# Kernel optimization log

Measured on AMD Instinct MI355X. Metric: run time of the kernel, lower is better.

Reference implementation:

```python
import jax, jax.numpy as jnp
import numpy as np

S = 1            # support_num
NEIGHBOR = 32    # neighbor_num for ball query
EPS = 1e-12

def _gather(t, idx):
    # t: (bs, N, C), idx: (bs, M, n) -> (bs, M, n, C)
    return jax.vmap(lambda tb, ib: tb[ib])(t, idx)

def _pick(t, idx):
    # t: (bs, M, C), idx: (bs, V) -> (bs, V, C)
    return jax.vmap(lambda tb, ib: tb[ib])(t, idx)

def _normalize(x, axis):
    return x / jnp.maximum(jnp.linalg.norm(x, axis=axis, keepdims=True), EPS)

def query_ball_point(radius, nsample, xyz, new_xyz):
    # PointNet++-style ball query: indices of first nsample points within radius,
    # missing slots filled with the first valid neighbor (self, since dist=0).
    sq = jnp.sum((new_xyz[:, :, None, :] - xyz[:, None, :, :]) ** 2, axis=-1)  # (bs,S,N)
    N = xyz.shape[1]
    idx = jnp.broadcast_to(jnp.arange(N), sq.shape)
    idx = jnp.where(sq > radius * radius, N, idx)
    idx = jnp.sort(idx, axis=-1)[:, :, :nsample]
    return jnp.where(idx == N, idx[:, :, :1], idx)

def _dir_norm(vertices, nbr_idx):
    nbrs = _gather(vertices, nbr_idx)                       # (bs,v,n,3)
    return _normalize(nbrs - vertices[:, :, None, :], axis=-1)

def conv_surface(nbr_idx, vertices, directions, K=32):
    # directions: (3, S*K)
    dn = _dir_norm(vertices, nbr_idx)
    theta = jax.nn.relu(jnp.einsum('bvnd,dk->bvnk', dn, _normalize(directions, 0)))
    bs, v, n, _ = theta.shape
    return theta.reshape(bs, v, n, S, K).max(axis=2).sum(axis=2)  # (bs,v,K)

def conv_layer(nbr_idx, vertices, fm, w, b, d, K=32):
    # w: (Cin,(S+1)*K), b: ((S+1)*K,), d: (3,S*K)
    dn = _dir_norm(vertices, nbr_idx)
    theta = jax.nn.relu(jnp.einsum('bvnd,dk->bvnk', dn, _normalize(d, 0)))  # (bs,v,n,S*K)
    f = jnp.einsum('bvc,ck->bvk', fm, w) + b                # (bs,v,(S+1)*K)
    center, support = f[..., :K], f[..., K:]
    sup = _gather(support, nbr_idx)                          # (bs,v,n,S*K)
    bs, v, n, _ = sup.shape
    act = (theta * sup).reshape(bs, v, n, S, K).max(axis=2).sum(axis=2)
    return center + act

def pool_layer(vertices, fm, radius, key, rate=4, nn_num=4):
    idx = query_ball_point(radius, nn_num, vertices, vertices)
    pooled = _gather(fm, idx).max(axis=2)                    # neighborhood max-pool
    v = vertices.shape[1]
    perm = jax.random.permutation(key, v)[: v // rate]       # random subsample (fixed key)
    return vertices[:, perm], pooled[:, perm]

def get_nearest_index(target, source):
    sq = jnp.sum((target[:, :, None, :] - source[:, None, :, :]) ** 2, axis=-1)
    return jnp.argmin(sq, axis=-1)                           # (bs, V_target)

def _forward(vertices, onehot, d0, w1, b1, dd1, w2, b2, dd2, w3, b3, dd3,
             w4, b4, dd4, w5, b5, dd5, w6, b6, dd6, w7, b7, dd7,
             cw1, cb1, cw2, cb2, cw3, cb3):
    relu = jax.nn.relu
    bs, V, _ = vertices.shape
    ni = query_ball_point(0.25, NEIGHBOR, vertices, vertices)
    fm0 = relu(conv_surface(ni, vertices, d0))
    fm1 = jnp.concatenate([fm0, relu(conv_layer(ni, vertices, fm0, w1, b1, dd1))], -1)
    fm2 = jnp.concatenate([fm1, relu(conv_layer(ni, vertices, fm1, w2, b2, dd2))], -1)
    v1, fp1 = pool_layer(vertices, fm2, 0.25, jax.random.fold_in(jax.random.key(42), 1))
    ni = query_ball_point(0.39, NEIGHBOR, v1, v1)
    fm3 = jnp.concatenate([fp1, relu(conv_layer(ni, v1, fp1, w3, b3, dd3))], -1)
    fm4 = jnp.concatenate([fm3, relu(conv_layer(ni, v1, fm3, w4, b4, dd4))], -1)
    fm5 = jnp.concatenate([fm4, relu(conv_layer(ni, v1, fm4, w5, b5, dd5))], -1)
    v2, fp2 = pool_layer(v1, fm5, 0.39, jax.random.fold_in(jax.random.key(42), 2))
    ni = query_ball_point(0.63, NEIGHBOR, v2, v2)
    fm6 = jnp.concatenate([fp2, relu(conv_layer(ni, v2, fp2, w6, b6, dd6))], -1)
    fm7 = jnp.concatenate([fm6, relu(conv_layer(ni, v2, fm6, w7, b7, dd7))], -1)
    f_global = fm7.max(axis=1)                               # (bs, 256)
    n1 = get_nearest_index(vertices, v1)
    n2 = get_nearest_index(vertices, v2)
    fuse = jnp.concatenate([
        fm0, fm1, fm2,
        _pick(fm3, n1), _pick(fm4, n1), _pick(fm5, n1),
        _pick(fm6, n2), _pick(fm7, n2),
        jnp.broadcast_to(f_global[:, None, :], (bs, V, f_global.shape[-1])),
        jnp.broadcast_to(onehot[:, None, :], (bs, V, onehot.shape[-1])),
    ], axis=-1)                                              # (bs, V, 1424)
    h = relu(jnp.einsum('bvc,oc->bvo', fuse, cw1) + cb1)
    h = relu(jnp.einsum('bvc,oc->bvo', h, cw2) + cb2)
    return jnp.einsum('bvc,oc->bvo', h, cw3) + cb3           # (bs, V, class_num)


def setup_inputs() -> dict:
    key = jax.random.key(0)
    ks = iter(jax.random.split(key, 40))
    bs, N, cat = 8, 2048, 16
    vertices = jax.random.uniform(next(ks), (bs, N, 3), dtype=jnp.float32)
    labels = jax.random.randint(next(ks), (bs,), 0, cat)
    onehot = jax.nn.one_hot(labels, cat, dtype=jnp.float32)
    def p(shape):
        return jax.random.normal(next(ks), shape, dtype=jnp.float32) * 0.05
    inp = {"vertices": vertices, "onehot": onehot, "d0": p((3, S * 32))}
    ins = [32, 64, 96, 128, 160, 192, 224]
    for i, c in enumerate(ins, start=1):
        inp[f"w{i}"] = p((c, (S + 1) * 32))
        inp[f"b{i}"] = p(((S + 1) * 32,))
        inp[f"dd{i}"] = p((3, S * 32))
    inp["cw1"] = p((1024, 1424)); inp["cb1"] = p((1024,))
    inp["cw2"] = p((512, 1024)); inp["cb2"] = p((512,))
    inp["cw3"] = p((50, 512)); inp["cb3"] = p((50,))
    return inp


def reference(vertices, onehot, d0, w1, b1, dd1, w2, b2, dd2, w3, b3, dd3,
              w4, b4, dd4, w5, b5, dd5, w6, b6, dd6, w7, b7, dd7,
              cw1, cb1, cw2, cb2, cw3, cb3):
    return _forward(vertices, onehot, d0, w1, b1, dd1, w2, b2, dd2, w3, b3, dd3,
                    w4, b4, dd4, w5, b5, dd5, w6, b6, dd6, w7, b7, dd7,
                    cw1, cb1, cw2, cb2, cw3, cb3)
```

## Files before the change

### kernel.cpp

```cpp
#include <hip/hip_runtime.h>
#include <hip/hip_bf16.h>

#define BS 8
#define V0 2048
#define V1N 512
#define V2N 128

typedef unsigned short ushort_t;
typedef __attribute__((ext_vector_type(8))) short bf16x8;
typedef __attribute__((ext_vector_type(4))) float f32x4;

__device__ __forceinline__ void tf2x32(unsigned k0, unsigned k1,
                                       unsigned x0, unsigned x1,
                                       unsigned &o0, unsigned &o1) {
  unsigned ks2 = k0 ^ k1 ^ 0x1BD11BDAu;
  x0 += k0; x1 += k1;
#define RR(r) { x0 += x1; x1 = (x1 << (r)) | (x1 >> (32 - (r))); x1 ^= x0; }
  RR(13) RR(15) RR(26) RR(6)   x0 += k1;  x1 += ks2 + 1u;
  RR(17) RR(29) RR(16) RR(24)  x0 += ks2; x1 += k0 + 2u;
  RR(13) RR(15) RR(26) RR(6)   x0 += k0;  x1 += k1 + 3u;
  RR(17) RR(29) RR(16) RR(24)  x0 += k1;  x1 += ks2 + 4u;
  RR(13) RR(15) RR(26) RR(6)   x0 += ks2; x1 += k0 + 5u;
#undef RR
  o0 = x0; o1 = x1;
}

__device__ __forceinline__ ushort_t f2bf(float f) {
  unsigned u = __float_as_uint(f);
  u += 0x7FFFu + ((u >> 16) & 1u);
  return (ushort_t)(u >> 16);
}

__device__ __forceinline__ float sqdist_f32(float cx, float cy, float cz,
                                            const float* p) {
  float dx = __fsub_rn(cx, p[0]);
  float dy = __fsub_rn(cy, p[1]);
  float dz = __fsub_rn(cz, p[2]);
  return __fadd_rn(__fadd_rn(__fmul_rn(dx, dx), __fmul_rn(dy, dy)),
                   __fmul_rn(dz, dz));
}

#define KP1 1472

#define PREP_BLKS 8193
__global__ __launch_bounds__(256) void misc1_kernel(
    int* __restrict__ rank, const float* __restrict__ cw1,
    const float* __restrict__ cw2, const float* __restrict__ cw3,
    const float* __restrict__ cb3, ushort_t* __restrict__ cw1b,
    ushort_t* __restrict__ cw2b, ushort_t* __restrict__ cw3b,
    float* __restrict__ cb3p, const float* __restrict__ pts,
    int* __restrict__ ni1) {
  int bid = blockIdx.x, tid = threadIdx.x;
  if (bid < 18) {
    __shared__ unsigned sb[2048];
    int seg, segfirst, n, base;
    if (bid < 8)       { seg = 0; segfirst = 0;  n = 2048; base = 0; }
    else if (bid < 16) { seg = 1; segfirst = 8;  n = 2048; base = 2048; }
    else               { seg = 2; segfirst = 16; n = 512;  base = 4096; }
    unsigned k0, k1, nk0, nk1, sk0, sk1;
    if (seg == 0) {
      tf2x32(0u, 42u, 0u, 1u, k0, k1);
      tf2x32(k0, k1, 0u, 1u, sk0, sk1);
    } else if (seg == 1) {
      tf2x32(0u, 42u, 0u, 1u, k0, k1);
      tf2x32(k0, k1, 0u, 0u, nk0, nk1);
      tf2x32(nk0, nk1, 0u, 1u, sk0, sk1);
    } else {
      tf2x32(0u, 42u, 0u, 2u, k0, k1);
      tf2x32(k0, k1, 0u, 1u, sk0, sk1);
    }
    for (int i = tid; i < n; i += 256) {
      unsigned o0, o1;
      tf2x32(sk0, sk1, 0u, (unsigned)i, o0, o1);
      sb[i] = o0 ^ o1;
    }
    __syncthreads();
    int tt = (bid - segfirst) * 256 + tid;
    unsigned bt = sb[tt];
    int cnt = 0;
#pragma unroll 8
    for (int s = 0; s < n; ++s) {
      unsigned bs = sb[s];
      cnt += (bs < bt) || (bs == bt && s < tt);
    }
    rank[base + tt] = cnt;
  } else if (bid < 18 + PREP_BLKS) {
    long long t = (long long)(bid - 18) * 256 + tid;
    const long long N1 = 1024LL * KP1, N2 = 512LL * 1024, N3 = 128LL * 512;
    if (t < N1) {
      int k = (int)(t % KP1);
      int n = (int)(t / KP1);
      cw1b[t] = f2bf(k < 1424 ? cw1[(size_t)n * 1424 + k] : 0.f);
    } else if (t < N1 + N2) {
      long long u = t - N1;
      cw2b[u] = f2bf(cw2[u]);
    } else if (t < N1 + N2 + N3) {
      long long u = t - N1 - N2;
      int k = (int)(u & 511);
      int n = (int)(u >> 9);
      cw3b[u] = f2bf(n < 50 ? cw3[(size_t)n * 512 + k] : 0.f);
    } else if (t < N1 + N2 + N3 + 128) {
      int u = (int)(t - N1 - N2 - N3);
      cb3p[u] = u < 50 ? cb3[u] : 0.f;
    }
  } else {
    int bq = bid - 18 - PREP_BLKS;
    int wid = bq * 4 + (tid >> 6);
    int lane = tid & 63;
    int b = wid >> 11, i = wid & 2047;
    const float* base = pts + (size_t)b * V0 * 3;
    float cx = base[i * 3], cy = base[i * 3 + 1], cz = base[i * 3 + 2];
    int cnt = 0, idx0 = 0;
    for (int j0 = 0; j0 < V0; j0 += 64) {
      int j = j0 + lane;
      float d2 = sqdist_f32(cx, cy, cz, base + (size_t)j * 3);
      bool in = (d2 <= 0.0625f);
      unsigned long long mask = __ballot(in);
      if (cnt == 0 && mask) idx0 = j0 + __builtin_ctzll(mask);
      if (in) {
        int rk = cnt + __popcll(mask & ((1ull << lane) - 1ull));
        if (rk < 32) ni1[(size_t)wid * 32 + rk] = j;
      }
      cnt += __popcll(mask);
      if (cnt >= 32) break;
    }
    for (int s = cnt + lane; s < 32; s += 64) ni1[(size_t)wid * 32 + s] = idx0;
  }
}

__device__ __forceinline__ void dirn(const float* base, int v, int nb,
                                     float& ox, float& oy, float& oz) {
  float dx = __fsub_rn(base[nb * 3 + 0], base[v * 3 + 0]);
  float dy = __fsub_rn(base[nb * 3 + 1], base[v * 3 + 1]);
  float dz = __fsub_rn(base[nb * 3 + 2], base[v * 3 + 2]);
  float s2 = __fadd_rn(__fadd_rn(__fmul_rn(dx, dx), __fmul_rn(dy, dy)),
                       __fmul_rn(dz, dz));
  float nrm = fmaxf(__fsqrt_rn(s2), 1e-12f);
  ox = __fdiv_rn(dx, nrm); oy = __fdiv_rn(dy, nrm); oz = __fdiv_rn(dz, nrm);
}

__device__ __forceinline__ void norm_col(const float* d, int k,
                                         float& ox, float& oy, float& oz) {
  float x = d[k], y = d[32 + k], z = d[64 + k];
  float s2 = __fadd_rn(__fadd_rn(__fmul_rn(x, x), __fmul_rn(y, y)),
                       __fmul_rn(z, z));
  float nrm = fmaxf(__fsqrt_rn(s2), 1e-12f);
  ox = __fdiv_rn(x, nrm); oy = __fdiv_rn(y, nrm); oz = __fdiv_rn(z, nrm);
}

__global__ __launch_bounds__(256) void misc2_kernel(
    const int* __restrict__ rank, int* __restrict__ perm1,
    int* __restrict__ perm2, const float* __restrict__ pts,
    const int* __restrict__ ni, const float* __restrict__ d0,
    const float* __restrict__ w1, const float* __restrict__ b1,
    float* __restrict__ out, float* __restrict__ fn) {
  int bid = blockIdx.x, tid = threadIdx.x;
  if (bid == 0) {
    __shared__ int a1[2048];
    __shared__ int a2[2048];
    for (int i = tid; i < 2048; i += 256) a1[rank[i]] = i;
    __syncthreads();
    for (int i = tid; i < 2048; i += 256) a2[rank[2048 + i]] = a1[i];
    __syncthreads();
    for (int i = tid; i < 512; i += 256) perm1[i] = a2[i];
    for (int i = tid; i < 512; i += 256) a1[rank[4096 + i]] = i;
    __syncthreads();
    for (int i = tid; i < 128; i += 256) perm2[i] = a1[i];
    return;
  }
  __shared__ float sdir[3][32];
  __shared__ float sdn[8][32][3];
  __shared__ float sfm[8][32];
  if (tid < 32) {
    float x, y, z; norm_col(d0, tid, x, y, z);
    sdir[0][tid] = x; sdir[1][tid] = y; sdir[2][tid] = z;
  }
  int vloc = tid >> 5, k = tid & 31;
  size_t bvg = (size_t)(bid - 1) * 8 + vloc;
  int b = (int)(bvg >> 11), v = (int)(bvg & 2047);
  const float* base = pts + (size_t)b * V0 * 3;
  int nb = ni[bvg * 32 + k];
  float x, y, z; dirn(base, v, nb, x, y, z);
  sdn[vloc][k][0] = x; sdn[vloc][k][1] = y; sdn[vloc][k][2] = z;
  __syncthreads();
  float m = 0.f;
  for (int n = 0; n < 32; ++n) {
    float d = sdn[vloc][n][0] * sdir[0][k] + sdn[vloc][n][1] * sdir[1][k] +
              sdn[vloc][n][2] * sdir[2][k];
    m = fmaxf(m, fmaxf(d, 0.f));
  }
  out[bvg * 96 + k] = m;
  sfm[vloc][k] = m;
  __syncthreads();
  float a1v = b1[k], a2v = b1[k + 32];
  for (int c = 0; c < 32; ++c) {
    float vv = sfm[vloc][c];
    a1v += vv * w1[c * 64 + k];
    a2v += vv * w1[c * 64 + k + 32];
  }
  fn[bvg * 64 + k] = a1v;
  fn[bvg * 64 + k + 32] = a2v;
}

__global__ __launch_bounds__(256) void conv_act_kernel(
    const float* __restrict__ pts, const float* __restrict__ dd,
    const int* __restrict__ ni, const float* __restrict__ f,
    float* __restrict__ out, int Nv, int ldout, int colofs,
    const float* __restrict__ wn, const float* __restrict__ bn,
    float* __restrict__ fn) {
  __shared__ float sdir[3][32];
  __shared__ float sdn[8][32][3];
  __shared__ int sidx[8][32];
  __shared__ float sfm[8][256];
  int tid = threadIdx.x;
  if (tid < 32) {
    float x, y, z; norm_col(dd, tid, x, y, z);
    sdir[0][tid] = x; sdir[1][tid] = y; sdir[2][tid] = z;
  }
  int vloc = tid >> 5, k = tid & 31;
  size_t bvg = (size_t)blockIdx.x * 8 + vloc;
  int b = (int)(bvg / Nv), v = (int)(bvg % Nv);
  const float* base = pts + (size_t)b * Nv * 3;
  int nb = ni[bvg * 32 + k];
  float x, y, z; dirn(base, v, nb, x, y, z);
  sdn[vloc][k][0] = x; sdn[vloc][k][1] = y; sdn[vloc][k][2] = z;
  sidx[vloc][k] = nb;
  __syncthreads();
  float m = -INFINITY;
  size_t fb = (size_t)b * Nv * 64;
  for (int n = 0; n < 32; ++n) {
    float th = fmaxf(sdn[vloc][n][0] * sdir[0][k] + sdn[vloc][n][1] * sdir[1][k] +
                     sdn[vloc][n][2] * sdir[2][k], 0.f);
    float sup = f[fb + (size_t)sidx[vloc][n] * 64 + 32 + k];
    m = fmaxf(m, th * sup);
  }
  float center = f[bvg * 64 + k];
  float res = fmaxf(center + m, 0.f);
  out[bvg * ldout + colofs + k] = res;
  if (wn) {
    size_t rowbase = (size_t)blockIdx.x * 8;
#pragma unroll 1
    for (int r = 0; r < 8; ++r)
      if (tid < colofs) sfm[r][tid] = out[(rowbase + r) * ldout + tid];
    sfm[vloc][colofs + k] = res;
    __syncthreads();
    int cin = colofs + 32;
    float a1v = bn[k], a2v = bn[k + 32];
    for (int c = 0; c < cin; ++c) {
      float vv = sfm[vloc][c];
      a1v += vv * wn[c * 64 + k];
      a2v += vv * wn[c * 64 + k + 32];
    }
    fn[bvg * 64 + k] = a1v;
    fn[bvg * 64 + k + 32] = a2v;
  }
}

__global__ __launch_bounds__(256) void conv_act_qbp_kernel(
    const float* __restrict__ pts, int Nv, float rrq,
    const float* __restrict__ dd, int* __restrict__ ni_out,
    const float* __restrict__ f, float* __restrict__ out, int ldout,
    int colofs, const float* __restrict__ wn, const float* __restrict__ bn,
    float* __restrict__ fn) {
  __shared__ float spts[512 * 3];
  __shared__ float sdir[3][32];
  __shared__ float sdn[8][32][3];
  __shared__ int sni[8][32];
  __shared__ float sfm[8][256];
  int tid = threadIdx.x;
  int b = (blockIdx.x * 8) / Nv;
  int vbase = (blockIdx.x * 8) % Nv;
  const float* gp = pts + (size_t)b * Nv * 3;
  for (int i = tid; i < Nv * 3; i += 256) spts[i] = gp[i];
  if (tid < 32) {
    float x, y, z; norm_col(dd, tid, x, y, z);
    sdir[0][tid] = x; sdir[1][tid] = y; sdir[2][tid] = z;
  }
  __syncthreads();
  int lane = tid & 63, wv = tid >> 6;
  for (int rep = 0; rep < 2; ++rep) {
    int vl = wv * 2 + rep;
    int v = vbase + vl;
    float cx = spts[v * 3], cy = spts[v * 3 + 1], cz = spts[v * 3 + 2];
    int cnt = 0, idx0 = 0;
    for (int j0 = 0; j0 < Nv; j0 += 64) {
      int j = j0 + lane;
      float d2 = sqdist_f32(cx, cy, cz, spts + (size_t)j * 3);
      bool in = (d2 <= rrq);
      unsigned long long mask = __ballot(in);
      if (cnt == 0 && mask) idx0 = j0 + __builtin_ctzll(mask);
      if (in) {
        int rk = cnt + __popcll(mask & ((1ull << lane) - 1ull));
        if (rk < 32) sni[vl][rk] = j;
      }
      cnt += __popcll(mask);
      if (cnt >= 32) break;
    }
    for (int s = cnt + lane; s < 32; s += 64) sni[vl][s] = idx0;
  }
  __syncthreads();
  ni_out[(size_t)(blockIdx.x * 8) * 32 + tid] = sni[tid >> 5][tid & 31];
  int vloc = tid >> 5, k = tid & 31;
  size_t bvg = (size_t)blockIdx.x * 8 + vloc;
  int v = vbase + vloc;
  int nb = sni[vloc][k];
  float x, y, z; dirn(spts, v, nb, x, y, z);
  sdn[vloc][k][0] = x; sdn[vloc][k][1] = y; sdn[vloc][k][2] = z;
  __syncthreads();
  float m = -INFINITY;
  size_t fb = (size_t)b * Nv * 64;
  for (int n = 0; n < 32; ++n) {
    float th = fmaxf(sdn[vloc][n][0] * sdir[0][k] + sdn[vloc][n][1] * sdir[1][k] +
                     sdn[vloc][n][2] * sdir[2][k], 0.f);
    float sup = f[fb + (size_t)sni[vloc][n] * 64 + 32 + k];
    m = fmaxf(m, th * sup);
  }
  float center = f[bvg * 64 + k];
  float res = fmaxf(center + m, 0.f);
  out[bvg * ldout + colofs + k] = res;
  size_t rowbase = (size_t)blockIdx.x * 8;
#pragma unroll 1
  for (int r = 0; r < 8; ++r)
    if (tid < colofs) sfm[r][tid] = out[(rowbase + r) * ldout + tid];
  sfm[vloc][colofs + k] = res;
  __syncthreads();
  int cin = colofs + 32;
  float a1v = bn[k], a2v = bn[k + 32];
  for (int c = 0; c < cin; ++c) {
    float vv = sfm[vloc][c];
    a1v += vv * wn[c * 64 + k];
    a2v += vv * wn[c * 64 + k + 32];
  }
  fn[bvg * 64 + k] = a1v;
  fn[bvg * 64 + k + 32] = a2v;
}

__global__ __launch_bounds__(256) void pool_kernel(
    const float* __restrict__ pts_in, const float* __restrict__ fm_in,
    int ld_in, int C, int Nv_in, const int* __restrict__ perm, int Nv_out,
    float rr, float* __restrict__ pts_out, float* __restrict__ fm_out,
    int ld_out, const float* __restrict__ wn, const float* __restrict__ bn,
    float* __restrict__ fn) {
  __shared__ float spf[4][192];
  int wv = threadIdx.x >> 6;
  int lane = threadIdx.x & 63;
  int wid = blockIdx.x * 4 + wv;
  int b = wid / Nv_out, pp = wid - b * Nv_out;
  int v = perm[pp];
  const float* base = pts_in + (size_t)b * Nv_in * 3;
  float cx = base[v * 3], cy = base[v * 3 + 1], cz = base[v * 3 + 2];
  int nb[4]; int cnt = 0;
  for (int j0 = 0; j0 < Nv_in && cnt < 4; j0 += 64) {
    int j = j0 + lane;
    float d2 = sqdist_f32(cx, cy, cz, base + (size_t)j * 3);
    unsigned long long mask = __ballot(d2 <= rr);
    while (mask && cnt < 4) {
      int bp = __builtin_ctzll(mask);
      mask &= mask - 1;
      nb[cnt++] = j0 + bp;
    }
  }
  for (int q = cnt; q < 4; ++q) nb[q] = nb[0];
  if (lane < 3) pts_out[(size_t)wid * 3 + lane] = base[v * 3 + lane];
  size_t inrow = (size_t)b * Nv_in;
  size_t outrow = (size_t)wid * ld_out;
  for (int c = lane; c < C; c += 64) {
    float m = fm_in[(inrow + nb[0]) * ld_in + c];
    m = fmaxf(m, fm_in[(inrow + nb[1]) * ld_in + c]);
    m = fmaxf(m, fm_in[(inrow + nb[2]) * ld_in + c]);
    m = fmaxf(m, fm_in[(inrow + nb[3]) * ld_in + c]);
    fm_out[outrow + c] = m;
    spf[wv][c] = m;
  }
  __syncthreads();
  int o = threadIdx.x & 63, w_ = threadIdx.x >> 6;
  int wid0 = blockIdx.x * 4 + w_;
  float a = bn[o];
  for (int c = 0; c < C; ++c) a += spf[w_][c] * wn[c * 64 + o];
  fn[(size_t)wid0 * 64 + o] = a;
}

__global__ void gmax_kernel(const float* __restrict__ fm,
                            float* __restrict__ out) {
  int t = blockIdx.x * blockDim.x + threadIdx.x;
  if (t >= BS * 256) return;
  int b = t >> 8, c = t & 255;
  float m = -INFINITY;
  for (int v = 0; v < V2N; ++v)
    m = fmaxf(m, fm[((size_t)b * V2N + v) * 256 + c]);
  out[t] = m;
}

__global__ __launch_bounds__(256) void fuse_row_kernel(
    const float* __restrict__ fm2, const float* __restrict__ fm5,
    const float* __restrict__ fm7, const float* __restrict__ fglob,
    const float* __restrict__ onehot, const float* __restrict__ verts,
    const float* __restrict__ v1, const float* __restrict__ v2,
    ushort_t* __restrict__ fuse_b) {
  __shared__ unsigned long long red[256];
  __shared__ int sn1, sn2;
  int bv = blockIdx.x;
  int b = bv >> 11;
  int tid = threadIdx.x;
  float cx = verts[(size_t)bv * 3 + 0];
  float cy = verts[(size_t)bv * 3 + 1];
  float cz = verts[(size_t)bv * 3 + 2];
  unsigned long long best = ~0ull;
  const float* sb = v1 + (size_t)b * V1N * 3;
  for (int j = tid; j < V1N; j += 256) {
    float d2 = sqdist_f32(cx, cy, cz, sb + (size_t)j * 3);
    unsigned long long key =
        (((unsigned long long)__float_as_uint(d2)) << 32) | (unsigned)j;
    best = best < key ? best : key;
  }
  red[tid] = best;
  __syncthreads();
  for (int s = 128; s > 0; s >>= 1) {
    if (tid < s) red[tid] = red[tid] < red[tid + s] ? red[tid] : red[tid + s];
    __syncthreads();
  }
  if (tid == 0) sn1 = (int)(red[0] & 0xffffffffu);
  __syncthreads();
  best = ~0ull;
  sb = v2 + (size_t)b * V2N * 3;
  for (int j = tid; j < V2N; j += 256) {
    float d2 = sqdist_f32(cx, cy, cz, sb + (size_t)j * 3);
    unsigned long long key =
        (((unsigned long long)__float_as_uint(d2)) << 32) | (unsigned)j;
    best = best < key ? best : key;
  }
  red[tid] = best;
  __syncthreads();
  for (int s = 128; s > 0; s >>= 1) {
    if (tid < s) red[tid] = red[tid] < red[tid + s] ? red[tid] : red[tid + s];
    __syncthreads();
  }
  if (tid == 0) sn2 = (int)(red[0] & 0xffffffffu);
  __syncthreads();
  const float* r2 = fm2 + (size_t)bv * 96;
  const float* r5 = fm5 + ((size_t)b * V1N + sn1) * 192;
  const float* r7 = fm7 + ((size_t)b * V2N + sn2) * 256;
  const float* rg = fglob + b * 256;
  const float* roh = onehot + b * 16;
  if (tid < KP1 / 8) {
    int c = tid * 8;
    const float* src = nullptr;
    if (c < 192) {
      int cc = (c < 32) ? c : (c < 96 ? c - 32 : c - 96);
      src = r2 + cc;
    } else if (c < 672) {
      int cc = (c < 320) ? c - 192 : (c < 480 ? c - 320 : c - 480);
      src = r5 + cc;
    } else if (c < 1152) {
      int cc = (c < 896) ? c - 672 : c - 896;
      src = r7 + cc;
    } else if (c < 1408) {
      src = rg + (c - 1152);
    } else if (c < 1424) {
      src = roh + (c - 1408);
    }
    float4 lo = make_float4(0.f, 0.f, 0.f, 0.f), hi = lo;
    if (src) { lo = *(const float4*)src; hi = *(const float4*)(src + 4); }
    bf16x8 o;
    o[0] = (short)f2bf(lo.x); o[1] = (short)f2bf(lo.y);
    o[2] = (short)f2bf(lo.z); o[3] = (short)f2bf(lo.w);
    o[4] = (short)f2bf(hi.x); o[5] = (short)f2bf(hi.y);
    o[6] = (short)f2bf(hi.z); o[7] = (short)f2bf(hi.w);
    *(bf16x8*)(fuse_b + (size_t)bv * KP1 + c) = o;
  }
}

typedef const __attribute__((address_space(1))) unsigned int gas_u32;
typedef __attribute__((address_space(3))) unsigned int las_u32;

__global__ __launch_bounds__(256) void gemm_mfma_nt(
    const ushort_t* __restrict__ A, const ushort_t* __restrict__ B,
    const float* __restrict__ bias, ushort_t* __restrict__ Cb,
    float* __restrict__ Cf, int K, int ldc, int nvalid, int mode) {
  __shared__ ushort_t As[128 * 64];
  __shared__ ushort_t Bs[128 * 64];
  int tid = threadIdx.x;
  int lane = tid & 63, w = tid >> 6;
  int wm = (w >> 1) * 64, wn = (w & 1) * 64;
  int nb = gridDim.x;
  int flat = blockIdx.x + nb * blockIdx.y;
  int xcd = flat & 7, slot = flat >> 3;
  int nidx = slot % nb;
  int mband = xcd + 8 * (slot / nb);
  int bm = mband * 128, bn = nidx * 128;
  f32x4 acc[4][4];
#pragma unroll
  for (int i = 0; i < 4; ++i)
#pragma unroll
    for (int j = 0; j < 4; ++j) acc[i][j] = (f32x4){0.f, 0.f, 0.f, 0.f};

  const ushort_t* gA[4];
  const ushort_t* gB[4];
  ushort_t* lA[4];
  ushort_t* lB[4];
  int rsub = lane >> 3;
  int scol = ((lane & 7) ^ rsub) * 8;
#pragma unroll
  for (int g = 0; g < 4; ++g) {
    int r = w * 32 + g * 8 + rsub;
    gA[g] = A + (size_t)(bm + r) * K + scol;
    gB[g] = B + (size_t)(bn + r) * K + scol;
    lA[g] = As + (w * 32 + g * 8) * 64;
    lB[g] = Bs + (w * 32 + g * 8) * 64;
  }
  int rA = lane & 15, q = lane >> 4;
  int r7 = rA & 7;

  for (int k0 = 0; k0 < K; k0 += 64) {
#pragma unroll
    for (int g = 0; g < 4; ++g)
      __builtin_amdgcn_global_load_lds((gas_u32*)(gA[g] + k0), (las_u32*)lA[g],
                                       16, 0, 0);
#pragma unroll
    for (int g = 0; g < 4; ++g)
      __builtin_amdgcn_global_load_lds((gas_u32*)(gB[g] + k0), (las_u32*)lB[g],
                                       16, 0, 0);
    __syncthreads();
#pragma unroll
    for (int s = 0; s < 2; ++s) {
      int pc = ((s * 4 + q) ^ r7) * 8;
      bf16x8 af[4], bfr[4];
#pragma unroll
      for (int i = 0; i < 4; ++i)
        af[i] = *(const bf16x8*)(As + (wm + i * 16 + rA) * 64 + pc);
#pragma unroll
      for (int j = 0; j < 4; ++j)
        bfr[j] = *(const bf16x8*)(Bs + (wn + j * 16 + rA) * 64 + pc);
#pragma unroll
      for (int i = 0; i < 4; ++i)
#pragma unroll
        for (int j = 0; j < 4; ++j)
          acc[i][j] = __builtin_amdgcn_mfma_f32_16x16x32_bf16(af[i], bfr[j],
                                                              acc[i][j], 0, 0, 0);
    }
    __syncthreads();
  }

  int rowq = (lane >> 4) * 4;
  int coll = lane & 15;
#pragma unroll
  for (int i = 0; i < 4; ++i) {
#pragma unroll
    for (int j = 0; j < 4; ++j) {
      int col = bn + wn + j * 16 + coll;
      float bi = bias[col];
#pragma unroll
      for (int r = 0; r < 4; ++r) {
        int row = bm + wm + i * 16 + rowq + r;
        float v = acc[i][j][r] + bi;
        if (mode == 0) {
          Cb[(size_t)row * ldc + col] = f2bf(fmaxf(v, 0.f));
        } else if (col < nvalid) {
          Cf[(size_t)row * ldc + col] = v;
        }
      }
    }
  }
}

extern "C" void kernel_launch(void* const* d_in, const int* in_sizes, int n_in,
                              void* d_out, int out_size, void* d_ws,
                              size_t ws_size, hipStream_t stream) {
  const float* vertices = (const float*)d_in[0];
  const float* onehot = (const float*)d_in[1];
  const float* d0 = (const float*)d_in[2];
  const float *w[8], *bb[8], *dd[8];
  for (int i = 1; i <= 7; ++i) {
    w[i] = (const float*)d_in[3 * i];
    bb[i] = (const float*)d_in[3 * i + 1];
    dd[i] = (const float*)d_in[3 * i + 2];
  }
  const float* cw1 = (const float*)d_in[24];
  const float* cb1 = (const float*)d_in[25];
  const float* cw2 = (const float*)d_in[26];
  const float* cb2 = (const float*)d_in[27];
  const float* cw3 = (const float*)d_in[28];
  const float* cb3 = (const float*)d_in[29];
  float* out = (float*)d_out;

  char* wsp = (char*)d_ws;
  size_t off = 0;
  auto alloc = [&](size_t bytes) -> void* {
    void* p = wsp + off;
    off += (bytes + 255) & ~(size_t)255;
    return p;
  };
  const int M = BS * V0;
  int* rank = (int*)alloc(4608 * 4);
  int* perm1 = (int*)alloc(512 * 4);
  int* perm2 = (int*)alloc(128 * 4);
  int* ni1 = (int*)alloc((size_t)BS * V0 * 32 * 4);
  int* ni2 = (int*)alloc((size_t)BS * V1N * 32 * 4);
  int* ni3 = (int*)alloc((size_t)BS * V2N * 32 * 4);
  float* fm2buf = (float*)alloc((size_t)BS * V0 * 96 * 4);
  float* fm5buf = (float*)alloc((size_t)BS * V1N * 192 * 4);
  float* fm7buf = (float*)alloc((size_t)BS * V2N * 256 * 4);
  float* fbuf = (float*)alloc((size_t)BS * V0 * 64 * 4);
  float* v1 = (float*)alloc((size_t)BS * V1N * 3 * 4);
  float* v2 = (float*)alloc((size_t)BS * V2N * 3 * 4);
  float* fglob = (float*)alloc((size_t)BS * 256 * 4);
  ushort_t* fuse_b = (ushort_t*)alloc((size_t)M * KP1 * 2);
  ushort_t* h1b = (ushort_t*)alloc((size_t)M * 1024 * 2);
  ushort_t* h2b = (ushort_t*)alloc((size_t)M * 512 * 2);
  ushort_t* cw1b = (ushort_t*)alloc((size_t)1024 * KP1 * 2);
  ushort_t* cw2b = (ushort_t*)alloc((size_t)512 * 1024 * 2);
  ushort_t* cw3b = (ushort_t*)alloc((size_t)128 * 512 * 2);
  float* cb3p = (float*)alloc(128 * 4);

  float rr1 = 0.0625f;
  float rr2 = (float)(0.39 * 0.39);
  float rr3 = (float)(0.63 * 0.63);

  misc1_kernel<<<18 + PREP_BLKS + 4096, 256, 0, stream>>>(
      rank, cw1, cw2, cw3, cb3, cw1b, cw2b, cw3b, cb3p, vertices, ni1);
  misc2_kernel<<<1 + BS * V0 / 8, 256, 0, stream>>>(
      rank, perm1, perm2, vertices, ni1, d0, w[1], bb[1], fm2buf, fbuf);
  conv_act_kernel<<<BS * V0 / 8, 256, 0, stream>>>(
      vertices, dd[1], ni1, fbuf, fm2buf, V0, 96, 32, w[2], bb[2], fbuf);
  conv_act_kernel<<<BS * V0 / 8, 256, 0, stream>>>(
      vertices, dd[2], ni1, fbuf, fm2buf, V0, 96, 64, nullptr, nullptr, nullptr);
  pool_kernel<<<BS * V1N / 4, 256, 0, stream>>>(
      vertices, fm2buf, 96, 96, V0, perm1, V1N, rr1, v1, fm5buf, 192,
      w[3], bb[3], fbuf);
  conv_act_qbp_kernel<<<BS * V1N / 8, 256, 0, stream>>>(
      v1, V1N, rr2, dd[3], ni2, fbuf, fm5buf, 192, 96, w[4], bb[4], fbuf);
  conv_act_kernel<<<BS * V1N / 8, 256, 0, stream>>>(
      v1, dd[4], ni2, fbuf, fm5buf, V1N, 192, 128, w[5], bb[5], fbuf);
  conv_act_kernel<<<BS * V1N / 8, 256, 0, stream>>>(
      v1, dd[5], ni2, fbuf, fm5buf, V1N, 192, 160, nullptr, nullptr, nullptr);
  pool_kernel<<<BS * V2N / 4, 256, 0, stream>>>(
      v1, fm5buf, 192, 192, V1N, perm2, V2N, rr2, v2, fm7buf, 256,
      w[6], bb[6], fbuf);
  conv_act_qbp_kernel<<<BS * V2N / 8, 256, 0, stream>>>(
      v2, V2N, rr3, dd[6], ni3, fbuf, fm7buf, 256, 192, w[7], bb[7], fbuf);
  conv_act_kernel<<<BS * V2N / 8, 256, 0, stream>>>(
      v2, dd[7], ni3, fbuf, fm7buf, V2N, 256, 224, nullptr, nullptr, nullptr);
  gmax_kernel<<<BS, 256, 0, stream>>>(fm7buf, fglob);
  fuse_row_kernel<<<M, 256, 0, stream>>>(fm2buf, fm5buf, fm7buf, fglob, onehot,
                                         vertices, v1, v2, fuse_b);
  gemm_mfma_nt<<<dim3(1024 / 128, M / 128), 256, 0, stream>>>(
      fuse_b, cw1b, cb1, h1b, nullptr, KP1, 1024, 1024, 0);
  gemm_mfma_nt<<<dim3(512 / 128, M / 128), 256, 0, stream>>>(
      h1b, cw2b, cb2, h2b, nullptr, 1024, 512, 512, 0);
  gemm_mfma_nt<<<dim3(1, M / 128), 256, 0, stream>>>(
      h2b, cw3b, cb3p, nullptr, out, 512, 50, 50, 1);
}
```

Baseline: 429.1 us.

## Use 256x256-tile 512-thread MFMA GEMM with XCD-aware block mapping for first FC layer

After: 416.0 us. 1.03x faster.

```diff
diff --git a/kernel.cpp b/kernel.cpp
--- a/kernel.cpp
+++ b/kernel.cpp
@@ -558,6 +558,137 @@
         } else if (col < nvalid) {
           Cf[(size_t)row * ldc + col] = v;
         }
+      }
+    }
+  }
+}
+
+__global__ __launch_bounds__(512, 2) void gemm256_mfma_nt(
+    const ushort_t* __restrict__ A, const ushort_t* __restrict__ B,
+    const float* __restrict__ bias, ushort_t* __restrict__ Cb,
+    int K, int ldc) {
+  __shared__ ushort_t As[2 * 256 * 64];
+  __shared__ ushort_t Bs[2 * 256 * 64];
+  int tid = threadIdx.x;
+  int lane = tid & 63, w = tid >> 6;
+  int wm = (w >> 2) * 128, wn = (w & 3) * 64;
+
+  int flat = blockIdx.x;
+  int xcd = flat & 7, slot = flat >> 3;
+  int nidx = slot & 3, mband = xcd + 8 * (slot >> 2);
+  int bm = mband * 256, bn = nidx * 256;
+
+  f32x4 acc[8][4];
+#pragma unroll
+  for (int i = 0; i < 8; ++i)
+#pragma unroll
+    for (int j = 0; j < 4; ++j) acc[i][j] = (f32x4){0.f, 0.f, 0.f, 0.f};
+
+  int rloc = tid >> 3, cch = tid & 7;
+  int gc = (cch ^ (rloc & 7)) * 8;
+  const ushort_t* gA[4];
+  const ushort_t* gB[4];
+#pragma unroll
+  for (int i = 0; i < 4; ++i) {
+    gA[i] = A + (size_t)(bm + i * 64 + rloc) * K + gc;
+    gB[i] = B + (size_t)(bn + i * 64 + rloc) * K + gc;
+  }
+  int lofs = tid * 8;
+
+  int rA = lane & 15, qlane = lane >> 4, r7 = lane & 7;
+  int pc0 = (qlane ^ r7) * 8;
+  int pc1 = ((4 + qlane) ^ r7) * 8;
+
+  int NT = K >> 6;
+
+#pragma unroll
+  for (int i = 0; i < 4; ++i) {
+    __builtin_amdgcn_global_load_lds((gas_u32*)gA[i],
+                                     (las_u32*)(As + i * 4096 + lofs), 16, 0, 0);
+    gA[i] += 64;
+  }
+#pragma unroll
+  for (int i = 0; i < 4; ++i) {
+    __builtin_amdgcn_global_load_lds((gas_u32*)gB[i],
+                                     (las_u32*)(Bs + i * 4096 + lofs), 16, 0, 0);
+    gB[i] += 64;
+  }
+
+  for (int t = 0; t < NT; ++t) {
+    int doff = (t & 1) * 16384;
+    int poff = doff ^ 16384;
+    if (t + 1 < NT) {
+#pragma unroll
+      for (int i = 0; i < 4; ++i) {
+        __builtin_amdgcn_global_load_lds(
+            (gas_u32*)gA[i], (las_u32*)(As + poff + i * 4096 + lofs), 16, 0, 0);
+        gA[i] += 64;
+      }
+#pragma unroll
+      for (int i = 0; i < 4; ++i) {
+        __builtin_amdgcn_global_load_lds(
+            (gas_u32*)gB[i], (las_u32*)(Bs + poff + i * 4096 + lofs), 16, 0, 0);
+        gB[i] += 64;
+      }
+      asm volatile("s_waitcnt vmcnt(8)" ::: "memory");
+    } else {
+      asm volatile("s_waitcnt vmcnt(0)" ::: "memory");
+    }
+    __builtin_amdgcn_sched_barrier(0);
+    __builtin_amdgcn_s_barrier();
+    __builtin_amdgcn_sched_barrier(0);
+
+    const ushort_t* Ab = As + doff;
+    const ushort_t* Bb = Bs + doff;
+#pragma unroll
+    for (int qd = 0; qd < 4; ++qd) {
+      int qrow = (qd >> 1) * 64, qcol = (qd & 1) * 32;
+      bf16x8 afr[2][4], bfr[2][2];
+#pragma unroll
+      for (int s = 0; s < 2; ++s) {
+        int pcs = s ? pc1 : pc0;
+#pragma unroll
+        for (int fi = 0; fi < 4; ++fi)
+          afr[s][fi] =
+              *(const bf16x8*)(Ab + (wm + qrow + fi * 16 + rA) * 64 + pcs);
+#pragma unroll
+        for (int fj = 0; fj < 2; ++fj)
+          bfr[s][fj] =
+              *(const bf16x8*)(Bb + (wn + qcol + fj * 16 + rA) * 64 + pcs);
+      }
+      __builtin_amdgcn_s_setprio(1);
+#pragma unroll
+      for (int s = 0; s < 2; ++s)
+#pragma unroll
+        for (int fi = 0; fi < 4; ++fi)
+#pragma unroll
+          for (int fj = 0; fj < 2; ++fj) {
+            int i = (qd >> 1) * 4 + fi, j = (qd & 1) * 2 + fj;
+            acc[i][j] = __builtin_amdgcn_mfma_f32_16x16x32_bf16(
+                afr[s][fi], bfr[s][fj], acc[i][j], 0, 0, 0);
+          }
+      __builtin_amdgcn_s_setprio(0);
+      __builtin_amdgcn_sched_barrier(0);
+      __builtin_amdgcn_s_barrier();
+      __builtin_amdgcn_sched_barrier(0);
+    }
+  }
+
+  int rowq = (lane >> 4) * 4;
+  int coll = lane & 15;
+  float bi[4];
+#pragma unroll
+  for (int j = 0; j < 4; ++j) bi[j] = bias[bn + wn + j * 16 + coll];
+#pragma unroll
+  for (int i = 0; i < 8; ++i) {
+#pragma unroll
+    for (int j = 0; j < 4; ++j) {
+      int col = bn + wn + j * 16 + coll;
+#pragma unroll
+      for (int r = 0; r < 4; ++r) {
+        int row = bm + wm + i * 16 + rowq + r;
+        float v = acc[i][j][r] + bi[j];
+        Cb[(size_t)row * ldc + col] = f2bf(fmaxf(v, 0.f));
       }
     }
   }
@@ -643,8 +774,8 @@
   gmax_kernel<<<BS, 256, 0, stream>>>(fm7buf, fglob);
   fuse_row_kernel<<<M, 256, 0, stream>>>(fm2buf, fm5buf, fm7buf, fglob, onehot,
                                          vertices, v1, v2, fuse_b);
-  gemm_mfma_nt<<<dim3(1024 / 128, M / 128), 256, 0, stream>>>(
-      fuse_b, cw1b, cb1, h1b, nullptr, KP1, 1024, 1024, 0);
+  gemm256_mfma_nt<<<(M / 256) * (1024 / 256), 512, 0, stream>>>(
+      fuse_b, cw1b, cb1, h1b, KP1, 1024);
   gemm_mfma_nt<<<dim3(512 / 128, M / 128), 256, 0, stream>>>(
       h1b, cw2b, cb2, h2b, nullptr, 1024, 512, 512, 0);
   gemm_mfma_nt<<<dim3(1, M / 128), 256, 0, stream>>>(
```
